# Optimization experiments

Measured on AMD Instinct MI355X. Metric: run time of the kernel, lower is better.

Reference implementation:

```python
import jax, jax.numpy as jnp
import numpy as np

B, T, DL, DM, H = 8, 4096, 1024, 1024, 8
HD = min(DL, DM) // H  # 128


def setup_inputs() -> dict:
    key = jax.random.key(0)
    ks = jax.random.split(key, 8)
    s = 0.02

    def w(k, shape):
        return jax.random.normal(k, shape, jnp.float32) * s

    return {
        "liquid_repr": jax.random.normal(ks[0], (B, T, DL), jnp.float32),
        "mamba_repr": jax.random.normal(ks[1], (B, T, DM), jnp.float32),
        "Wlq": w(ks[2], (DL, H * HD)), "blq": jnp.zeros((H * HD,), jnp.float32),
        "Wmkv": w(ks[3], (DM, 2 * H * HD)), "bmkv": jnp.zeros((2 * H * HD,), jnp.float32),
        "Wmq": w(ks[4], (DM, H * HD)), "bmq": jnp.zeros((H * HD,), jnp.float32),
        "Wlkv": w(ks[5], (DL, 2 * H * HD)), "blkv": jnp.zeros((2 * H * HD,), jnp.float32),
        "Wlo": w(ks[6], (H * HD, DL)), "blo": jnp.zeros((DL,), jnp.float32),
        "Wmo": w(ks[7], (H * HD, DM)), "bmo": jnp.zeros((DM,), jnp.float32),
    }


def _attn(q, k, v):
    # q,k,v: [B,T,H,HD]. Faithful to torch: matmul over last two dims ->
    # scores [B,T,H,H] (attention over the heads axis per timestep).
    scores = jnp.einsum('bthd,btgd->bthg', q, k) / jnp.sqrt(jnp.float32(HD))
    w = jax.nn.softmax(scores, axis=-1)
    return jnp.einsum('bthg,btgd->bthd', w, v)


def reference(liquid_repr, mamba_repr, Wlq, blq, Wmkv, bmkv, Wmq, bmq,
              Wlkv, blkv, Wlo, blo, Wmo, bmo):
    b, t, _ = liquid_repr.shape
    # liquid queries mamba
    q_l = (liquid_repr @ Wlq + blq).reshape(b, t, H, HD)
    kv_m = (mamba_repr @ Wmkv + bmkv).reshape(b, t, H, 2 * HD)
    k_m, v_m = kv_m[..., :HD], kv_m[..., HD:]
    a_l = _attn(q_l, k_m, v_m).reshape(b, t, H * HD)
    enhanced_liquid = liquid_repr + a_l @ Wlo + blo
    # mamba queries liquid
    q_m = (mamba_repr @ Wmq + bmq).reshape(b, t, H, HD)
    kv_l = (liquid_repr @ Wlkv + blkv).reshape(b, t, H, 2 * HD)
    k_l, v_l = kv_l[..., :HD], kv_l[..., HD:]
    a_m = _attn(q_m, k_l, v_l).reshape(b, t, H * HD)
    enhanced_mamba = mamba_repr + a_m @ Wmo + bmo
    return enhanced_liquid, enhanced_mamba
```

## Files before the change

kernel.cpp:

```cpp
#include <hip/hip_runtime.h>

typedef unsigned short u16;
typedef unsigned int u32;

typedef __attribute__((ext_vector_type(4))) float floatx4;
typedef __attribute__((ext_vector_type(8))) __bf16 bf16x8;

typedef __attribute__((address_space(3))) u32 lds_u32_t;
typedef __attribute__((address_space(1))) u32 glb_u32_t;

__device__ __forceinline__ void gld_lds16(const u16* g, u16* l) {
    __builtin_amdgcn_global_load_lds((glb_u32_t*)g, (lds_u32_t*)l, 16, 0, 0);
}

__device__ __forceinline__ u16 f2bf(float f) {
    u32 u = __float_as_uint(f);
    u += 0x7fffu + ((u >> 16) & 1u);
    return (u16)(u >> 16);
}
__device__ __forceinline__ u32 pk2(float a, float b) {
    u32 x = __float_as_uint(a), y = __float_as_uint(b);
    x += 0x7fffu + ((x >> 16) & 1u);
    y += 0x7fffu + ((y >> 16) & 1u);
    return (x >> 16) | (y & 0xffff0000u);
}

#define SWZ(d) ((d) ^ ((((d) >> 7) & 7) << 4))

#define BM 128
#define BN 128
#define BK 64

__global__ __launch_bounds__(256) void convert_f32_bf16(
    const float* __restrict__ src, u16* __restrict__ dst)
{
    const size_t i = ((size_t)blockIdx.x * 256 + threadIdx.x) * 8;
    float4 a = *(const float4*)(src + i);
    float4 b = *(const float4*)(src + i + 4);
    *(uint4*)(dst + i) = make_uint4(pk2(a.x, a.y), pk2(a.z, a.w),
                                    pk2(b.x, b.y), pk2(b.z, b.w));
}

__global__ __launch_bounds__(256, 2) void gemm_a16_c16(
    const u16* __restrict__ A, int lda,
    const u16* __restrict__ Bt,
    const float* __restrict__ bias,
    u16* __restrict__ C, int ldc,
    int K)
{
    __shared__ __align__(16) u16 sA[BM * BK];
    __shared__ __align__(16) u16 sB[BN * BK];
    const int tid  = threadIdx.x;
    const int bm   = blockIdx.x, bn = blockIdx.y;
    const int lane = tid & 63,  wave = tid >> 6;
    const int wm   = wave >> 1, wn   = wave & 1;
    const int l15  = lane & 15, quad = lane >> 4;
    const char* sAb = (const char*)sA;
    const char* sBb = (const char*)sB;

    floatx4 acc[4][4] = {};

    for (int k0 = 0; k0 < K; k0 += BK) {
        __syncthreads();
#pragma unroll
        for (int j = 0; j < 4; ++j) {
            const int clin = tid + j * 256;
            const int csrc = clin ^ ((clin >> 3) & 7);
            const int r = csrc >> 3, c = (csrc & 7) * 8;
            gld_lds16(A  + (size_t)(bm * BM + r) * lda + k0 + c, &sA[clin * 8]);
            gld_lds16(Bt + (size_t)(bn * BN + r) * K   + k0 + c, &sB[clin * 8]);
        }
        __syncthreads();

#pragma unroll
        for (int ks = 0; ks < 2; ++ks) {
            bf16x8 af[4], bfr[4];
#pragma unroll
            for (int mi = 0; mi < 4; mi++)
                af[mi] = *(const bf16x8*)(sAb +
                    SWZ((wm * 64 + mi * 16 + l15) * 128 + ks * 64 + quad * 16));
#pragma unroll
            for (int ni = 0; ni < 4; ni++)
                bfr[ni] = *(const bf16x8*)(sBb +
                    SWZ((wn * 64 + ni * 16 + l15) * 128 + ks * 64 + quad * 16));
#pragma unroll
            for (int mi = 0; mi < 4; mi++)
#pragma unroll
                for (int ni = 0; ni < 4; ni++)
                    acc[mi][ni] = __builtin_amdgcn_mfma_f32_16x16x32_bf16(
                        af[mi], bfr[ni], acc[mi][ni], 0, 0, 0);
        }
    }

    const int row0 = bm * BM + wm * 64 + quad * 4;
    const int col0 = bn * BN + wn * 64 + l15;
#pragma unroll
    for (int mi = 0; mi < 4; mi++) {
#pragma unroll
        for (int ni = 0; ni < 4; ni++) {
            const int col = col0 + ni * 16;
            const float bv = bias[col];
#pragma unroll
            for (int r = 0; r < 4; r++) {
                const int row = row0 + mi * 16 + r;
                C[(size_t)row * ldc + col] = f2bf(acc[mi][ni][r] + bv);
            }
        }
    }
}

__global__ __launch_bounds__(256, 2) void gemm_a16_c32(
    const u16* __restrict__ A, int lda,
    const u16* __restrict__ Bt,
    const float* __restrict__ bias,
    const float* __restrict__ R, int ldr,
    float* __restrict__ C, int ldc,
    int K)
{
    __shared__ __align__(16) u16 sA[BM * BK];
    __shared__ __align__(16) u16 sB[BN * BK];
    const int tid  = threadIdx.x;
    const int bm   = blockIdx.x, bn = blockIdx.y;
    const int lane = tid & 63,  wave = tid >> 6;
    const int wm   = wave >> 1, wn   = wave & 1;
    const int l15  = lane & 15, quad = lane >> 4;
    const char* sAb = (const char*)sA;
    const char* sBb = (const char*)sB;

    floatx4 acc[4][4] = {};

    for (int k0 = 0; k0 < K; k0 += BK) {
        __syncthreads();
#pragma unroll
        for (int j = 0; j < 4; ++j) {
            const int clin = tid + j * 256;
            const int csrc = clin ^ ((clin >> 3) & 7);
            const int r = csrc >> 3, c = (csrc & 7) * 8;
            gld_lds16(A  + (size_t)(bm * BM + r) * lda + k0 + c, &sA[clin * 8]);
            gld_lds16(Bt + (size_t)(bn * BN + r) * K   + k0 + c, &sB[clin * 8]);
        }
        __syncthreads();

#pragma unroll
        for (int ks = 0; ks < 2; ++ks) {
            bf16x8 af[4], bfr[4];
#pragma unroll
            for (int mi = 0; mi < 4; mi++)
                af[mi] = *(const bf16x8*)(sAb +
                    SWZ((wm * 64 + mi * 16 + l15) * 128 + ks * 64 + quad * 16));
#pragma unroll
            for (int ni = 0; ni < 4; ni++)
                bfr[ni] = *(const bf16x8*)(sBb +
                    SWZ((wn * 64 + ni * 16 + l15) * 128 + ks * 64 + quad * 16));
#pragma unroll
            for (int mi = 0; mi < 4; mi++)
#pragma unroll
                for (int ni = 0; ni < 4; ni++)
                    acc[mi][ni] = __builtin_amdgcn_mfma_f32_16x16x32_bf16(
                        af[mi], bfr[ni], acc[mi][ni], 0, 0, 0);
        }
    }

    const int row0 = bm * BM + wm * 64 + quad * 4;
    const int col0 = bn * BN + wn * 64 + l15;
#pragma unroll
    for (int mi = 0; mi < 4; mi++) {
#pragma unroll
        for (int ni = 0; ni < 4; ni++) {
            const int col = col0 + ni * 16;
            const float bv = bias[col];
#pragma unroll
            for (int r = 0; r < 4; r++) {
                const int row = row0 + mi * 16 + r;
                C[(size_t)row * ldc + col] =
                    acc[mi][ni][r] + bv + R[(size_t)row * ldr + col];
            }
        }
    }
}

#define AW 136

__global__ __launch_bounds__(256) void attn8(
    const u16* Q,
    const u16* __restrict__ KV,
    u16* O,
    int qstride, int kvstride)
{
    __shared__ __align__(16) float lds[4 * (3 * 8 * AW + 64)];
    const int wid = threadIdx.x >> 6, lane = threadIdx.x & 63;
    float* qs = lds + wid * (3 * 8 * AW + 64);
    float* ks = qs + 8 * AW;
    float* vs = ks + 8 * AW;
    float* ws = vs + 8 * AW;
    const size_t pos = (size_t)blockIdx.x * 4 + wid;
    const u16* qrow  = Q  + pos * qstride;
    const u16* kvrow = KV + pos * kvstride;

#pragma unroll
    for (int it = 0; it < 2; it++) {
        int vi = lane + 64 * it;
        int h = vi >> 4, c = (vi & 15) * 8;
        uint4 r = *(const uint4*)(qrow + vi * 8);
        float f0 = __uint_as_float(r.x << 16), f1 = __uint_as_float(r.x & 0xffff0000u);
        float f2 = __uint_as_float(r.y << 16), f3 = __uint_as_float(r.y & 0xffff0000u);
        float f4 = __uint_as_float(r.z << 16), f5 = __uint_as_float(r.z & 0xffff0000u);
        float f6 = __uint_as_float(r.w << 16), f7 = __uint_as_float(r.w & 0xffff0000u);
        float4* d = (float4*)&qs[h * AW + c];
        d[0] = make_float4(f0, f1, f2, f3);
        d[1] = make_float4(f4, f5, f6, f7);
    }
#pragma unroll
    for (int it = 0; it < 4; it++) {
        int vi = lane + 64 * it;
        int g = vi >> 5, c = (vi & 31) * 8;
        uint4 r = *(const uint4*)(kvrow + vi * 8);
        float f0 = __uint_as_float(r.x << 16), f1 = __uint_as_float(r.x & 0xffff0000u);
        float f2 = __uint_as_float(r.y << 16), f3 = __uint_as_float(r.y & 0xffff0000u);
        float f4 = __uint_as_float(r.z << 16), f5 = __uint_as_float(r.z & 0xffff0000u);
        float f6 = __uint_as_float(r.w << 16), f7 = __uint_as_float(r.w & 0xffff0000u);
        float* base = (c < 128) ? &ks[g * AW + c] : &vs[g * AW + (c - 128)];
        ((float4*)base)[0] = make_float4(f0, f1, f2, f3);
        ((float4*)base)[1] = make_float4(f4, f5, f6, f7);
    }
    __syncthreads();

    const int h = lane >> 3, g = lane & 7;
    float s = 0.f;
#pragma unroll 8
    for (int d = 0; d < 128; d += 4) {
        float4 qv = *(const float4*)&qs[h * AW + d];
        float4 kv = *(const float4*)&ks[g * AW + d];
        s += qv.x * kv.x + qv.y * kv.y + qv.z * kv.z + qv.w * kv.w;
    }
    s *= 0.08838834764831845f;
    float m = s;
    m = fmaxf(m, __shfl_xor(m, 1, 64));
    m = fmaxf(m, __shfl_xor(m, 2, 64));
    m = fmaxf(m, __shfl_xor(m, 4, 64));
    float p = __expf(s - m);
    float sum = p;
    sum += __shfl_xor(sum, 1, 64);
    sum += __shfl_xor(sum, 2, 64);
    sum += __shfl_xor(sum, 4, 64);
    ws[lane] = p / sum;
    __syncthreads();

    const int db = lane & 7;
    float o[16];
#pragma unroll
    for (int j = 0; j < 16; j++) o[j] = 0.f;
#pragma unroll
    for (int g2 = 0; g2 < 8; g2++) {
        float wv = ws[h * 8 + g2];
        const float* vr = &vs[g2 * AW + db * 16];
#pragma unroll
        for (int j = 0; j < 16; j++) o[j] += wv * vr[j];
    }
    u16* orow = O + pos * qstride + h * 128 + db * 16;
    u32 pk[8];
#pragma unroll
    for (int j = 0; j < 8; j++)
        pk[j] = (u32)f2bf(o[2 * j]) | ((u32)f2bf(o[2 * j + 1]) << 16);
    ((uint4*)orow)[0] = make_uint4(pk[0], pk[1], pk[2], pk[3]);
    ((uint4*)orow)[1] = make_uint4(pk[4], pk[5], pk[6], pk[7]);
}

__global__ __launch_bounds__(256) void transpose_f32_bf16(
    const float* __restrict__ src, u16* __restrict__ dst, int K, int N)
{
    __shared__ float tile[32][33];
    const int tx = threadIdx.x & 31, ty = threadIdx.x >> 5;
    const int c0 = blockIdx.x * 32, r0 = blockIdx.y * 32;
#pragma unroll
    for (int i = 0; i < 4; i++)
        tile[ty + i * 8][tx] = src[(size_t)(r0 + ty + i * 8) * N + c0 + tx];
    __syncthreads();
#pragma unroll
    for (int i = 0; i < 4; i++)
        dst[(size_t)(c0 + ty + i * 8) * K + r0 + tx] = f2bf(tile[tx][ty + i * 8]);
}

extern "C" void kernel_launch(void* const* d_in, const int* in_sizes, int n_in,
                              void* d_out, int out_size, void* d_ws, size_t ws_size,
                              hipStream_t stream) {
    const float* liquid = (const float*)d_in[0];
    const float* mamba  = (const float*)d_in[1];
    const float* Wlq  = (const float*)d_in[2];
    const float* blq  = (const float*)d_in[3];
    const float* Wmkv = (const float*)d_in[4];
    const float* bmkv = (const float*)d_in[5];
    const float* Wmq  = (const float*)d_in[6];
    const float* bmq  = (const float*)d_in[7];
    const float* Wlkv = (const float*)d_in[8];
    const float* blkv = (const float*)d_in[9];
    const float* Wlo  = (const float*)d_in[10];
    const float* blo  = (const float*)d_in[11];
    const float* Wmo  = (const float*)d_in[12];
    const float* bmo  = (const float*)d_in[13];
    float* out = (float*)d_out;

    u16* p = (u16*)d_ws;
    u16* WtLq  = p; p += (size_t)1024 * 1024;
    u16* WtLkv = p; p += (size_t)2048 * 1024;
    u16* WtMq  = p; p += (size_t)1024 * 1024;
    u16* WtMkv = p; p += (size_t)2048 * 1024;
    u16* WtLo  = p; p += (size_t)1024 * 1024;
    u16* WtMo  = p; p += (size_t)1024 * 1024;
    u16* Q  = p; p += (size_t)32768 * 1024;
    u16* KV = p;

    u16* Lb = (u16*)(out + (size_t)32768 * 1024);
    u16* Mb = Lb + (size_t)32768 * 1024;

    transpose_f32_bf16<<<dim3(32, 32), 256, 0, stream>>>(Wlq,  WtLq,  1024, 1024);
    transpose_f32_bf16<<<dim3(64, 32), 256, 0, stream>>>(Wlkv, WtLkv, 1024, 2048);
    transpose_f32_bf16<<<dim3(32, 32), 256, 0, stream>>>(Wmq,  WtMq,  1024, 1024);
    transpose_f32_bf16<<<dim3(64, 32), 256, 0, stream>>>(Wmkv, WtMkv, 1024, 2048);
    transpose_f32_bf16<<<dim3(32, 32), 256, 0, stream>>>(Wlo,  WtLo,  1024, 1024);
    transpose_f32_bf16<<<dim3(32, 32), 256, 0, stream>>>(Wmo,  WtMo,  1024, 1024);

    convert_f32_bf16<<<16384, 256, 0, stream>>>(liquid, Lb);
    convert_f32_bf16<<<16384, 256, 0, stream>>>(mamba,  Mb);

    gemm_a16_c16<<<dim3(256, 8),  256, 0, stream>>>(Lb, 1024, WtLq,  blq,  Q,  1024, 1024);
    gemm_a16_c16<<<dim3(256, 16), 256, 0, stream>>>(Mb, 1024, WtMkv, bmkv, KV, 2048, 1024);
    attn8<<<8192, 256, 0, stream>>>(Q, KV, Q, 1024, 2048);
    gemm_a16_c32<<<dim3(256, 8),  256, 0, stream>>>(Q, 1024, WtLo, blo, liquid, 1024,
                                                    out, 1024, 1024);

    gemm_a16_c16<<<dim3(256, 8),  256, 0, stream>>>(Mb, 1024, WtMq,  bmq,  Q,  1024, 1024);
    gemm_a16_c16<<<dim3(256, 16), 256, 0, stream>>>(Lb, 1024, WtLkv, blkv, KV, 2048, 1024);
    attn8<<<8192, 256, 0, stream>>>(Q, KV, Q, 1024, 2048);
    gemm_a16_c32<<<dim3(256, 8),  256, 0, stream>>>(Q, 1024, WtMo, bmo, mamba, 1024,
                                                    out + (size_t)32768 * 1024, 1024, 1024);
}
```

Measured before the change: 1.357 ms.

## Remap GEMM workgroups for XCD locality and make attention register-only

The GEMMs switch to a 1D grid with a remap that groups consecutive tiles onto the same XCD, taking blockIdx modulo 8 as the XCD index. Tiles that share A rows then run on one XCD and can hit its L2. The attention kernel drops LDS staging and syncthreads: each lane reads its q/k rows straight from global bf16, and the softmax weights are broadcast with shuffles. This adds redundant global loads (each q row is read by 8 lanes) in exchange for no LDS traffic and higher occupancy.

```diff
diff --git a/kernel.cpp b/kernel.cpp
--- a/kernel.cpp
+++ b/kernel.cpp
@@ -24,6 +24,8 @@
     y += 0x7fffu + ((y >> 16) & 1u);
     return (x >> 16) | (y & 0xffff0000u);
 }
+__device__ __forceinline__ float bl(u32 u) { return __uint_as_float(u << 16); }
+__device__ __forceinline__ float bh(u32 u) { return __uint_as_float(u & 0xffff0000u); }
 
 #define SWZ(d) ((d) ^ ((((d) >> 7) & 7) << 4))
 
@@ -41,17 +43,25 @@
                                     pk2(b.x, b.y), pk2(b.z, b.w));
 }
 
+__device__ __forceinline__ void remap_bmbn(int nbn, int& bm, int& bn) {
+    const int nwg = (int)gridDim.x;
+    const int flat = (int)blockIdx.x;
+    const int wg = (flat & 7) * (nwg >> 3) + (flat >> 3);
+    bn = wg % nbn;
+    bm = wg / nbn;
+}
+
 __global__ __launch_bounds__(256, 2) void gemm_a16_c16(
     const u16* __restrict__ A, int lda,
     const u16* __restrict__ Bt,
     const float* __restrict__ bias,
     u16* __restrict__ C, int ldc,
-    int K)
+    int K, int nbn)
 {
     __shared__ __align__(16) u16 sA[BM * BK];
     __shared__ __align__(16) u16 sB[BN * BK];
     const int tid  = threadIdx.x;
-    const int bm   = blockIdx.x, bn = blockIdx.y;
+    int bm, bn; remap_bmbn(nbn, bm, bn);
     const int lane = tid & 63,  wave = tid >> 6;
     const int wm   = wave >> 1, wn   = wave & 1;
     const int l15  = lane & 15, quad = lane >> 4;
@@ -115,12 +125,12 @@
     const float* __restrict__ bias,
     const float* __restrict__ R, int ldr,
     float* __restrict__ C, int ldc,
-    int K)
+    int K, int nbn)
 {
     __shared__ __align__(16) u16 sA[BM * BK];
     __shared__ __align__(16) u16 sB[BN * BK];
     const int tid  = threadIdx.x;
-    const int bm   = blockIdx.x, bn = blockIdx.y;
+    int bm, bn; remap_bmbn(nbn, bm, bn);
     const int lane = tid & 63,  wave = tid >> 6;
     const int wm   = wave >> 1, wn   = wave & 1;
     const int l15  = lane & 15, quad = lane >> 4;
@@ -179,61 +189,32 @@
     }
 }
 
-#define AW 136
-
 __global__ __launch_bounds__(256) void attn8(
     const u16* Q,
     const u16* __restrict__ KV,
     u16* O,
     int qstride, int kvstride)
 {
-    __shared__ __align__(16) float lds[4 * (3 * 8 * AW + 64)];
     const int wid = threadIdx.x >> 6, lane = threadIdx.x & 63;
-    float* qs = lds + wid * (3 * 8 * AW + 64);
-    float* ks = qs + 8 * AW;
-    float* vs = ks + 8 * AW;
-    float* ws = vs + 8 * AW;
     const size_t pos = (size_t)blockIdx.x * 4 + wid;
     const u16* qrow  = Q  + pos * qstride;
     const u16* kvrow = KV + pos * kvstride;
-
-#pragma unroll
-    for (int it = 0; it < 2; it++) {
-        int vi = lane + 64 * it;
-        int h = vi >> 4, c = (vi & 15) * 8;
-        uint4 r = *(const uint4*)(qrow + vi * 8);
-        float f0 = __uint_as_float(r.x << 16), f1 = __uint_as_float(r.x & 0xffff0000u);
-        float f2 = __uint_as_float(r.y << 16), f3 = __uint_as_float(r.y & 0xffff0000u);
-        float f4 = __uint_as_float(r.z << 16), f5 = __uint_as_float(r.z & 0xffff0000u);
-        float f6 = __uint_as_float(r.w << 16), f7 = __uint_as_float(r.w & 0xffff0000u);
-        float4* d = (float4*)&qs[h * AW + c];
-        d[0] = make_float4(f0, f1, f2, f3);
-        d[1] = make_float4(f4, f5, f6, f7);
-    }
-#pragma unroll
-    for (int it = 0; it < 4; it++) {
-        int vi = lane + 64 * it;
-        int g = vi >> 5, c = (vi & 31) * 8;
-        uint4 r = *(const uint4*)(kvrow + vi * 8);
-        float f0 = __uint_as_float(r.x << 16), f1 = __uint_as_float(r.x & 0xffff0000u);
-        float f2 = __uint_as_float(r.y << 16), f3 = __uint_as_float(r.y & 0xffff0000u);
-        float f4 = __uint_as_float(r.z << 16), f5 = __uint_as_float(r.z & 0xffff0000u);
-        float f6 = __uint_as_float(r.w << 16), f7 = __uint_as_float(r.w & 0xffff0000u);
-        float* base = (c < 128) ? &ks[g * AW + c] : &vs[g * AW + (c - 128)];
-        ((float4*)base)[0] = make_float4(f0, f1, f2, f3);
-        ((float4*)base)[1] = make_float4(f4, f5, f6, f7);
-    }
-    __syncthreads();
-
     const int h = lane >> 3, g = lane & 7;
-    float s = 0.f;
-#pragma unroll 8
-    for (int d = 0; d < 128; d += 4) {
-        float4 qv = *(const float4*)&qs[h * AW + d];
-        float4 kv = *(const float4*)&ks[g * AW + d];
-        s += qv.x * kv.x + qv.y * kv.y + qv.z * kv.z + qv.w * kv.w;
-    }
-    s *= 0.08838834764831845f;
+
+    const u16* qh = qrow  + h * 128;
+    const u16* kg = kvrow + g * 256;
+    float s0 = 0.f, s1 = 0.f, s2 = 0.f, s3 = 0.f;
+#pragma unroll
+    for (int j = 0; j < 16; ++j) {
+        uint4 qa = *(const uint4*)(qh + j * 8);
+        uint4 ka = *(const uint4*)(kg + j * 8);
+        s0 += bl(qa.x) * bl(ka.x);  s1 += bh(qa.x) * bh(ka.x);
+        s2 += bl(qa.y) * bl(ka.y);  s3 += bh(qa.y) * bh(ka.y);
+        s0 += bl(qa.z) * bl(ka.z);  s1 += bh(qa.z) * bh(ka.z);
+        s2 += bl(qa.w) * bl(ka.w);  s3 += bh(qa.w) * bh(ka.w);
+    }
+    float s = ((s0 + s1) + (s2 + s3)) * 0.08838834764831845f;
+
     float m = s;
     m = fmaxf(m, __shfl_xor(m, 1, 64));
     m = fmaxf(m, __shfl_xor(m, 2, 64));
@@ -243,25 +224,34 @@
     sum += __shfl_xor(sum, 1, 64);
     sum += __shfl_xor(sum, 2, 64);
     sum += __shfl_xor(sum, 4, 64);
-    ws[lane] = p / sum;
-    __syncthreads();
-
-    const int db = lane & 7;
+    const float w = p / sum;
+
+    const int db = g;
     float o[16];
 #pragma unroll
-    for (int j = 0; j < 16; j++) o[j] = 0.f;
-#pragma unroll
-    for (int g2 = 0; g2 < 8; g2++) {
-        float wv = ws[h * 8 + g2];
-        const float* vr = &vs[g2 * AW + db * 16];
-#pragma unroll
-        for (int j = 0; j < 16; j++) o[j] += wv * vr[j];
-    }
+    for (int j = 0; j < 16; ++j) o[j] = 0.f;
+    const u16* vbase = kvrow + 128 + db * 16;
+#pragma unroll
+    for (int gg = 0; gg < 8; ++gg) {
+        const float wv = __shfl(w, h * 8 + gg, 64);
+        const u16* vp = vbase + gg * 256;
+        uint4 va = *(const uint4*)(vp);
+        uint4 vb = *(const uint4*)(vp + 8);
+        o[0]  += wv * bl(va.x);  o[1]  += wv * bh(va.x);
+        o[2]  += wv * bl(va.y);  o[3]  += wv * bh(va.y);
+        o[4]  += wv * bl(va.z);  o[5]  += wv * bh(va.z);
+        o[6]  += wv * bl(va.w);  o[7]  += wv * bh(va.w);
+        o[8]  += wv * bl(vb.x);  o[9]  += wv * bh(vb.x);
+        o[10] += wv * bl(vb.y);  o[11] += wv * bh(vb.y);
+        o[12] += wv * bl(vb.z);  o[13] += wv * bh(vb.z);
+        o[14] += wv * bl(vb.w);  o[15] += wv * bh(vb.w);
+    }
+
     u16* orow = O + pos * qstride + h * 128 + db * 16;
     u32 pk[8];
 #pragma unroll
-    for (int j = 0; j < 8; j++)
-        pk[j] = (u32)f2bf(o[2 * j]) | ((u32)f2bf(o[2 * j + 1]) << 16);
+    for (int j = 0; j < 8; ++j)
+        pk[j] = pk2(o[2 * j], o[2 * j + 1]);
     ((uint4*)orow)[0] = make_uint4(pk[0], pk[1], pk[2], pk[3]);
     ((uint4*)orow)[1] = make_uint4(pk[4], pk[5], pk[6], pk[7]);
 }
@@ -323,15 +313,15 @@
     convert_f32_bf16<<<16384, 256, 0, stream>>>(liquid, Lb);
     convert_f32_bf16<<<16384, 256, 0, stream>>>(mamba,  Mb);
 
-    gemm_a16_c16<<<dim3(256, 8),  256, 0, stream>>>(Lb, 1024, WtLq,  blq,  Q,  1024, 1024);
-    gemm_a16_c16<<<dim3(256, 16), 256, 0, stream>>>(Mb, 1024, WtMkv, bmkv, KV, 2048, 1024);
+    gemm_a16_c16<<<2048, 256, 0, stream>>>(Lb, 1024, WtLq,  blq,  Q,  1024, 1024, 8);
+    gemm_a16_c16<<<4096, 256, 0, stream>>>(Mb, 1024, WtMkv, bmkv, KV, 2048, 1024, 16);
     attn8<<<8192, 256, 0, stream>>>(Q, KV, Q, 1024, 2048);
-    gemm_a16_c32<<<dim3(256, 8),  256, 0, stream>>>(Q, 1024, WtLo, blo, liquid, 1024,
-                                                    out, 1024, 1024);
-
-    gemm_a16_c16<<<dim3(256, 8),  256, 0, stream>>>(Mb, 1024, WtMq,  bmq,  Q,  1024, 1024);
-    gemm_a16_c16<<<dim3(256, 16), 256, 0, stream>>>(Lb, 1024, WtLkv, blkv, KV, 2048, 1024);
+    gemm_a16_c32<<<2048, 256, 0, stream>>>(Q, 1024, WtLo, blo, liquid, 1024,
+                                           out, 1024, 1024, 8);
+
+    gemm_a16_c16<<<2048, 256, 0, stream>>>(Mb, 1024, WtMq,  bmq,  Q,  1024, 1024, 8);
+    gemm_a16_c16<<<4096, 256, 0, stream>>>(Lb, 1024, WtLkv, blkv, KV, 2048, 1024, 16);
     attn8<<<8192, 256, 0, stream>>>(Q, KV, Q, 1024, 2048);
-    gemm_a16_c32<<<dim3(256, 8),  256, 0, stream>>>(Q, 1024, WtMo, bmo, mamba, 1024,
-                                                    out + (size_t)32768 * 1024, 1024, 1024);
-}
+    gemm_a16_c32<<<2048, 256, 0, stream>>>(Q, 1024, WtMo, bmo, mamba, 1024,
+                                           out + (size_t)32768 * 1024, 1024, 1024, 8);
+}
```

Measured after the change: 1.370 ms. About the same (+1.0%).
